# Optimization experiments

Hardware: AMD Instinct MI355X
Metric: run time of the kernel (lower is better)

The kernel has to match this reference:

```python
import jax, jax.numpy as jnp
import numpy as np

NUM_HEADS = 16
BLOCK_SIZE = 64
NUM_GLOBAL_TOKENS = 64
WINDOW_SIZE = 256
NUM_RANDOM_BLOCKS = 3
BATCH = 2
SEQ_LEN = 4096
EMBED_DIM = 1024


def _alibi_slopes(n):
    # power-of-2 head count path of _compute_alibi_slopes
    base = 2.0 ** (-(2.0 ** (-(np.log2(n) - 3.0))))
    return jnp.asarray([base ** i for i in range(1, n + 1)], dtype=jnp.float32)


def _build_block_indices():
    nb = SEQ_LEN // BLOCK_SIZE
    ngb = NUM_GLOBAL_TOKENS // BLOCK_SIZE
    wb = WINDOW_SIZE // BLOCK_SIZE
    mb = 2 * wb + 1 + NUM_RANDOM_BLOCKS
    rng = np.random.default_rng(0)
    out = np.full((nb, mb), -1, dtype=np.int64)
    for qb in range(nb):
        attended = set(range(ngb))  # global blocks handled separately
        idx = 0
        for kb in range(max(ngb, qb - wb), min(nb, qb + wb + 1)):
            if kb not in attended:
                out[qb, idx] = kb
                attended.add(kb)
                idx += 1
        cand = [b for b in range(ngb, nb) if b not in attended]
        pick = rng.choice(len(cand), size=min(NUM_RANDOM_BLOCKS, len(cand)), replace=False)
        for j in pick:
            out[qb, idx] = cand[j]
            idx += 1
    return jnp.asarray(out)


def setup_inputs() -> dict:
    key = jax.random.key(0)
    ks = jax.random.split(key, 5)
    s = 0.02
    x = jax.random.normal(ks[0], (BATCH, SEQ_LEN, EMBED_DIM), jnp.float32)
    Wq = jax.random.normal(ks[1], (EMBED_DIM, EMBED_DIM), jnp.float32) * s
    Wk = jax.random.normal(ks[2], (EMBED_DIM, EMBED_DIM), jnp.float32) * s
    Wv = jax.random.normal(ks[3], (EMBED_DIM, EMBED_DIM), jnp.float32) * s
    Wo = jax.random.normal(ks[4], (EMBED_DIM, EMBED_DIM), jnp.float32) * s
    return {"x": x, "Wq": Wq, "Wk": Wk, "Wv": Wv, "Wo": Wo,
            "block_indices": _build_block_indices()}


def reference(x, Wq, Wk, Wv, Wo, block_indices):
    B, S, E = x.shape
    H = NUM_HEADS
    Dh = E // H
    G = NUM_GLOBAL_TOKENS
    BS = BLOCK_SIZE
    scale = 1.0 / np.sqrt(Dh)

    def split_heads(t):
        return t.reshape(B, S, H, Dh).transpose(0, 2, 1, 3)  # [B,H,S,Dh]

    q = split_heads(x @ Wq)
    k = split_heads(x @ Wk)
    v = split_heads(x @ Wv)

    slopes = _alibi_slopes(H)  # [H]
    pos = jnp.arange(S, dtype=jnp.float32)

    # ---- global tokens: full attention over all keys ----
    sg = jnp.einsum('bhgd,bhsd->bhgs', q[:, :, :G], k) * scale
    bias_g = -slopes[:, None, None] * jnp.abs(pos[:G, None] - pos[None, :])  # [H,G,S]
    pg = jax.nn.softmax(sg + bias_g[None], axis=-1)
    out_g = jnp.einsum('bhgs,bhsd->bhgd', pg, v)  # [B,H,G,Dh]

    # ---- sparse queries: global KV + gathered sparse blocks ----
    nb = S // BS
    ngb = G // BS
    nqb = nb - ngb
    bi = block_indices[ngb:]           # [nqb, MB], -1 = padding
    mb = bi.shape[1]
    bsafe = jnp.maximum(bi, 0)

    kb = k.reshape(B, H, nb, BS, Dh)
    vb = v.reshape(B, H, nb, BS, Dh)
    kg = kb[:, :, bsafe].reshape(B, H, nqb, mb * BS, Dh)
    vg = vb[:, :, bsafe].reshape(B, H, nqb, mb * BS, Dh)
    kglob = jnp.broadcast_to(k[:, :, None, :G], (B, H, nqb, G, Dh))
    vglob = jnp.broadcast_to(v[:, :, None, :G], (B, H, nqb, G, Dh))
    kcat = jnp.concatenate([kglob, kg], axis=3)  # [B,H,nqb,G+mb*BS,Dh]
    vcat = jnp.concatenate([vglob, vg], axis=3)

    qn = q[:, :, G:].reshape(B, H, nqb, BS, Dh)
    scores = jnp.einsum('bhqmd,bhqnd->bhqmn', qn, kcat) * scale

    qpos = (G + jnp.arange(nqb * BS, dtype=jnp.float32)).reshape(nqb, BS)
    loc_pos = (bsafe[:, :, None] * BS + jnp.arange(BS)[None, None, :]).reshape(nqb, mb * BS).astype(jnp.float32)
    kpos = jnp.concatenate([jnp.broadcast_to(pos[:G][None], (nqb, G)), loc_pos], axis=1)
    bias = -slopes[:, None, None, None] * jnp.abs(qpos[None, :, :, None] - kpos[None, :, None, :])  # [H,nqb,BS,Kt]

    valid = jnp.concatenate([jnp.ones((nqb, G), bool), jnp.repeat(bi >= 0, BS, axis=1)], axis=1)
    scores = jnp.where(valid[None, None, :, None, :], scores + bias[None], -jnp.inf)
    p = jax.nn.softmax(scores, axis=-1)
    out_s = jnp.einsum('bhqmn,bhqnd->bhqmd', p, vcat).reshape(B, H, S - G, Dh)

    out = jnp.concatenate([out_g, out_s], axis=2)  # [B,H,S,Dh]
    out = out.transpose(0, 2, 1, 3).reshape(B, S, E)
    return out @ Wo
```

## Files before the change

### kernel.cpp

```cpp
#include <hip/hip_runtime.h>
#include <stdint.h>

typedef __attribute__((ext_vector_type(8))) short short8;
typedef __attribute__((ext_vector_type(4))) float f32x4;
typedef __attribute__((ext_vector_type(8))) unsigned short u16x8;

#define DEV static __device__ __forceinline__

DEV unsigned short f2bf(float f) {
  union { float f; uint32_t u; } v; v.f = f;
  uint32_t r = v.u + 0x7FFFu + ((v.u >> 16) & 1u);
  return (unsigned short)(r >> 16);
}

DEV void gload16(const void* g, void* l) {
  __builtin_amdgcn_global_load_lds(
      (const __attribute__((address_space(1))) void*)g,
      (__attribute__((address_space(3))) void*)l, 16, 0, 0);
}

__global__ void cast_x_kernel(const float* __restrict__ x, unsigned short* __restrict__ xb) {
  int i = blockIdx.x * 256 + threadIdx.x;
  f32x4 a = ((const f32x4*)x)[2 * i];
  f32x4 b = ((const f32x4*)x)[2 * i + 1];
  u16x8 o;
  o[0] = f2bf(a[0]); o[1] = f2bf(a[1]); o[2] = f2bf(a[2]); o[3] = f2bf(a[3]);
  o[4] = f2bf(b[0]); o[5] = f2bf(b[1]); o[6] = f2bf(b[2]); o[7] = f2bf(b[3]);
  ((u16x8*)xb)[i] = o;
}

__global__ void transpose_w_kernel(const float* __restrict__ Wq, const float* __restrict__ Wk,
                                   const float* __restrict__ Wv, const float* __restrict__ Wo,
                                   unsigned short* __restrict__ wt) {
  __shared__ float tile[64][65];
  int z = blockIdx.z;
  const float* W = (z == 0) ? Wq : (z == 1) ? Wk : (z == 2) ? Wv : Wo;
  unsigned short* dst = wt + (size_t)z * 1024 * 1024;
  int bn = blockIdx.x, bk = blockIdx.y;
  int t = threadIdx.x;
  int c = t & 63, rr = t >> 6;
#pragma unroll
  for (int p = 0; p < 16; ++p) {
    int r = p * 4 + rr;
    tile[r][c] = W[(size_t)(bk * 64 + r) * 1024 + bn * 64 + c];
  }
  __syncthreads();
#pragma unroll
  for (int p = 0; p < 16; ++p) {
    int r2 = p * 4 + rr;
    dst[(size_t)(bn * 64 + r2) * 1024 + bk * 64 + c] = f2bf(tile[c][r2]);
  }
}

__global__ __launch_bounds__(256, 2) void gemm_qkv(const unsigned short* __restrict__ A,
                                                   const unsigned short* __restrict__ wt,
                                                   unsigned short* __restrict__ Qb,
                                                   unsigned short* __restrict__ Kb,
                                                   unsigned short* __restrict__ Vtb,
                                                   float qscale) {
  constexpr int K = 1024;
  __shared__ __align__(16) unsigned short As[128 * 64];
  __shared__ __align__(16) unsigned short Bs[128 * 64];
  int bn = blockIdx.x, bm = blockIdx.y;
  int which = bn >> 3, bnn = bn & 7;
  int tid = threadIdx.x, lane = tid & 63, w = tid >> 6;
  int wr = w >> 1, wc = w & 1;
  f32x4 acc[4][4] = {};

  int sr[4], soff[4];
#pragma unroll
  for (int i = 0; i < 4; ++i) {
    int ci = w * 4 + i;
    int r = ci * 8 + (lane >> 3);
    sr[i] = r;
    soff[i] = ((lane & 7) ^ (r & 7)) * 8;
  }
  const unsigned short* Arow = A + (size_t)(bm * 128) * K;
  const unsigned short* Brow = wt + (size_t)which * 1048576 + (size_t)(bnn * 128) * K;

  for (int k0 = 0; k0 < K; k0 += 64) {
#pragma unroll
    for (int i = 0; i < 4; ++i) {
      gload16(Arow + (size_t)sr[i] * K + k0 + soff[i], As + (w * 4 + i) * 512);
      gload16(Brow + (size_t)sr[i] * K + k0 + soff[i], Bs + (w * 4 + i) * 512);
    }
    __syncthreads();
    short8 af[2][4], bfr[2][4];
#pragma unroll
    for (int c = 0; c < 2; ++c) {
#pragma unroll
      for (int m = 0; m < 4; ++m) {
        int cc = (lane >> 4) + 4 * c;
        int ra = wr * 64 + m * 16 + (lane & 15);
        af[c][m] = *(const short8*)(As + ra * 64 + ((cc ^ (ra & 7)) * 8));
        int rb = wc * 64 + m * 16 + (lane & 15);
        bfr[c][m] = *(const short8*)(Bs + rb * 64 + ((cc ^ (rb & 7)) * 8));
      }
    }
#pragma unroll
    for (int c = 0; c < 2; ++c)
#pragma unroll
      for (int m = 0; m < 4; ++m)
#pragma unroll
        for (int n = 0; n < 4; ++n)
          acc[m][n] = __builtin_amdgcn_mfma_f32_16x16x32_bf16(af[c][m], bfr[c][n], acc[m][n], 0, 0, 0);
    __syncthreads();
  }

  int rbase = bm * 128 + wr * 64;
  int cbase = bnn * 128 + wc * 64;
#pragma unroll
  for (int m = 0; m < 4; ++m)
#pragma unroll
    for (int n = 0; n < 4; ++n) {
      int row0 = rbase + m * 16 + (lane >> 4) * 4;
      int col = cbase + n * 16 + (lane & 15);
      int h = col >> 6, d = col & 63;
#pragma unroll
      for (int reg = 0; reg < 4; ++reg) {
        int row = row0 + reg;
        float v = acc[m][n][reg];
        int b = row >> 12, s = row & 4095;
        if (which == 0)
          Qb[((size_t)(b * 16 + h) * 4096 + s) * 64 + d] = f2bf(v * qscale);
        else if (which == 1)
          Kb[((size_t)(b * 16 + h) * 4096 + s) * 64 + d] = f2bf(v);
        else
          Vtb[(((size_t)(b * 16 + h) * 64 + (s >> 6)) * 64 + d) * 64 + (s & 63)] = f2bf(v);
      }
    }
}

__global__ __launch_bounds__(256, 2) void gemm_out(const unsigned short* __restrict__ A,
                                                   const unsigned short* __restrict__ Bt,
                                                   float* __restrict__ dst) {
  constexpr int K = 1024;
  __shared__ __align__(16) unsigned short As[128 * 64];
  __shared__ __align__(16) unsigned short Bs[128 * 64];
  int bn = blockIdx.x, bm = blockIdx.y;
  int tid = threadIdx.x, lane = tid & 63, w = tid >> 6;
  int wr = w >> 1, wc = w & 1;
  f32x4 acc[4][4] = {};

  int sr[4], soff[4];
#pragma unroll
  for (int i = 0; i < 4; ++i) {
    int ci = w * 4 + i;
    int r = ci * 8 + (lane >> 3);
    sr[i] = r;
    soff[i] = ((lane & 7) ^ (r & 7)) * 8;
  }
  const unsigned short* Arow = A + (size_t)(bm * 128) * K;
  const unsigned short* Brow = Bt + (size_t)(bn * 128) * K;

  for (int k0 = 0; k0 < K; k0 += 64) {
#pragma unroll
    for (int i = 0; i < 4; ++i) {
      gload16(Arow + (size_t)sr[i] * K + k0 + soff[i], As + (w * 4 + i) * 512);
      gload16(Brow + (size_t)sr[i] * K + k0 + soff[i], Bs + (w * 4 + i) * 512);
    }
    __syncthreads();
    short8 af[2][4], bfr[2][4];
#pragma unroll
    for (int c = 0; c < 2; ++c) {
#pragma unroll
      for (int m = 0; m < 4; ++m) {
        int cc = (lane >> 4) + 4 * c;
        int ra = wr * 64 + m * 16 + (lane & 15);
        af[c][m] = *(const short8*)(As + ra * 64 + ((cc ^ (ra & 7)) * 8));
        int rb = wc * 64 + m * 16 + (lane & 15);
        bfr[c][m] = *(const short8*)(Bs + rb * 64 + ((cc ^ (rb & 7)) * 8));
      }
    }
#pragma unroll
    for (int c = 0; c < 2; ++c)
#pragma unroll
      for (int m = 0; m < 4; ++m)
#pragma unroll
        for (int n = 0; n < 4; ++n)
          acc[m][n] = __builtin_amdgcn_mfma_f32_16x16x32_bf16(af[c][m], bfr[c][n], acc[m][n], 0, 0, 0);
    __syncthreads();
  }

  int rbase = bm * 128 + wr * 64;
  int cbase = bn * 128 + wc * 64;
#pragma unroll
  for (int m = 0; m < 4; ++m)
#pragma unroll
    for (int n = 0; n < 4; ++n) {
      int row0 = rbase + m * 16 + (lane >> 4) * 4;
      int col = cbase + n * 16 + (lane & 15);
#pragma unroll
      for (int reg = 0; reg < 4; ++reg)
        dst[(size_t)(row0 + reg) * 1024 + col] = acc[m][n][reg];
    }
}

__global__ __launch_bounds__(256) void attn_kernel(const unsigned short* __restrict__ Qh,
                            const unsigned short* __restrict__ Kh,
                            const unsigned short* __restrict__ Vbt,
                            const int* __restrict__ bidx,
                            unsigned short* __restrict__ attn_out,
                            float* __restrict__ Opart,
                            float* __restrict__ lpart) {
  __shared__ __align__(16) unsigned short Ks[2][64 * 64];
  __shared__ __align__(16) unsigned short Vs[2][64 * 64];
  __shared__ __align__(16) unsigned short Pl[2][4][16][72];
  int flat = blockIdx.x + 71 * blockIdx.y;
  int nf = (flat & 7) * 284 + (flat >> 3);
  int gx = nf % 71, bh = nf / 71;
  int h = bh & 15;
  int tid = threadIdx.x, lane = tid & 63, w = tid >> 6;
  float slope2 = exp2f(-0.5f * (float)(h + 1)) * 1.44269504f;

  int qb, nkb;
  int list[13];
  if (gx < 63) {
    qb = gx + 1;
    nkb = 1;
    list[0] = 0;
#pragma unroll
    for (int j = 0; j < 12; ++j) {
      int v = bidx[qb * 12 + j];
      if (v >= 0) list[nkb++] = v;
    }
  } else {
    qb = 0;
    int chunk = gx - 63;
    nkb = 8;
#pragma unroll
    for (int i = 0; i < 8; ++i) list[i] = chunk * 8 + i;
  }

  int qrow = qb * 64 + w * 16 + (lane & 15);
  const unsigned short* qptr = Qh + ((size_t)bh * 4096 + qrow) * 64 + (lane >> 4) * 8;
  short8 qf0 = *(const short8*)qptr;
  short8 qf1 = *(const short8*)(qptr + 32);

  float psum[4] = {0.f, 0.f, 0.f, 0.f};
  f32x4 accO[4] = {};
  int qpos0 = qb * 64 + w * 16 + (lane >> 4) * 4;

  float qposf[4], fm[4], fp[4], kctf[4];
#pragma unroll
  for (int reg = 0; reg < 4; ++reg) {
    qposf[reg] = (float)(qpos0 + reg);
    fm[reg] = -slope2 * qposf[reg];
    fp[reg] = slope2 * qposf[reg];
  }
#pragma unroll
  for (int ct = 0; ct < 4; ++ct) kctf[ct] = (float)(ct * 16 + (lane & 15));

  const unsigned short* Kbh = Kh + (size_t)bh * 4096 * 64;
  const unsigned short* Vbh = Vbt + (size_t)bh * 4096 * 64;

  int sr[2], so[2];
#pragma unroll
  for (int i = 0; i < 2; ++i) {
    int ci = w * 2 + i;
    int r = ci * 8 + (lane >> 3);
    sr[i] = r;
    so[i] = ((lane & 7) ^ (r & 7)) * 8;
  }
  auto STAGE = [&](int bi, int kb) {
    const unsigned short* kbase = Kbh + (size_t)kb * 4096;
    const unsigned short* vbase = Vbh + (size_t)kb * 4096;
#pragma unroll
    for (int i = 0; i < 2; ++i) {
      gload16(kbase + sr[i] * 64 + so[i], &Ks[bi][(w * 2 + i) * 512]);
      gload16(vbase + sr[i] * 64 + so[i], &Vs[bi][(w * 2 + i) * 512]);
    }
  };

  STAGE(0, list[0]);

  for (int it = 0; it < nkb; ++it) {
    int cur = it & 1;
    int kb = list[it];
    __syncthreads();
    if (it + 1 < nkb) STAGE(cur ^ 1, list[it + 1]);

    float kbf = (float)(kb * 64);
    float skb = slope2 * kbf;
    float pv[4][4];

    if (kb != qb) {
      float d_[4][4];
      if (kb < qb) {
#pragma unroll
        for (int ct = 0; ct < 4; ++ct) {
          float e = __builtin_fmaf(slope2, kctf[ct], skb);
#pragma unroll
          for (int reg = 0; reg < 4; ++reg) d_[ct][reg] = fm[reg] + e;
        }
      } else {
#pragma unroll
        for (int ct = 0; ct < 4; ++ct) {
          float e = __builtin_fmaf(slope2, kctf[ct], skb);
#pragma unroll
          for (int reg = 0; reg < 4; ++reg) d_[ct][reg] = fp[reg] - e;
        }
      }
      __builtin_amdgcn_s_setprio(1);
#pragma unroll
      for (int ct = 0; ct < 4; ++ct) {
        int kr = ct * 16 + (lane & 15);
        short8 kf0 = *(const short8*)(&Ks[cur][kr * 64 + (((lane >> 4) ^ (kr & 7)) * 8)]);
        short8 kf1 = *(const short8*)(&Ks[cur][kr * 64 + ((((lane >> 4) + 4) ^ (kr & 7)) * 8)]);
        f32x4 s = __builtin_amdgcn_mfma_f32_16x16x32_bf16(qf0, kf0, (f32x4){0.f, 0.f, 0.f, 0.f}, 0, 0, 0);
        s = __builtin_amdgcn_mfma_f32_16x16x32_bf16(qf1, kf1, s, 0, 0, 0);
#pragma unroll
        for (int reg = 0; reg < 4; ++reg) {
          float p = exp2f(s[reg] + d_[ct][reg]);
          pv[ct][reg] = p;
          psum[reg] += p;
        }
      }
      __builtin_amdgcn_s_setprio(0);
    } else {
      float qmb[4];
#pragma unroll
      for (int reg = 0; reg < 4; ++reg) qmb[reg] = qposf[reg] - kbf;
      __builtin_amdgcn_s_setprio(1);
#pragma unroll
      for (int ct = 0; ct < 4; ++ct) {
        int kr = ct * 16 + (lane & 15);
        short8 kf0 = *(const short8*)(&Ks[cur][kr * 64 + (((lane >> 4) ^ (kr & 7)) * 8)]);
        short8 kf1 = *(const short8*)(&Ks[cur][kr * 64 + ((((lane >> 4) + 4) ^ (kr & 7)) * 8)]);
        f32x4 s = __builtin_amdgcn_mfma_f32_16x16x32_bf16(qf0, kf0, (f32x4){0.f, 0.f, 0.f, 0.f}, 0, 0, 0);
        s = __builtin_amdgcn_mfma_f32_16x16x32_bf16(qf1, kf1, s, 0, 0, 0);
#pragma unroll
        for (int reg = 0; reg < 4; ++reg) {
          float diff = qmb[reg] - kctf[ct];
          float p = exp2f(__builtin_fmaf(-slope2, fabsf(diff), s[reg]));
          pv[ct][reg] = p;
          psum[reg] += p;
        }
      }
      __builtin_amdgcn_s_setprio(0);
    }

#pragma unroll
    for (int cp = 0; cp < 2; ++cp)
#pragma unroll
      for (int reg = 0; reg < 4; ++reg) {
        uint32_t pk;
        asm("v_cvt_pk_bf16_f32 %0, %1, %2" : "=v"(pk) : "v"(pv[2 * cp][reg]), "v"(pv[2 * cp + 1][reg]));
        int row = (lane >> 4) * 4 + reg;
        int c = lane & 15;
        Pl[cur][w][row][cp * 32 + c] = (unsigned short)pk;
        Pl[cur][w][row][cp * 32 + 16 + c] = (unsigned short)(pk >> 16);
      }

    asm volatile("s_waitcnt lgkmcnt(0)" ::: "memory");
    short8 pa0 = *(const short8*)(&Pl[cur][w][lane & 15][(lane >> 4) * 8]);
    short8 pa1 = *(const short8*)(&Pl[cur][w][lane & 15][(lane >> 4) * 8 + 32]);
    __builtin_amdgcn_s_setprio(1);
#pragma unroll
    for (int dt = 0; dt < 4; ++dt) {
      int dr = dt * 16 + (lane & 15);
      short8 vf0 = *(const short8*)(&Vs[cur][dr * 64 + (((lane >> 4) ^ (dr & 7)) * 8)]);
      short8 vf1 = *(const short8*)(&Vs[cur][dr * 64 + ((((lane >> 4) + 4) ^ (dr & 7)) * 8)]);
      accO[dt] = __builtin_amdgcn_mfma_f32_16x16x32_bf16(pa0, vf0, accO[dt], 0, 0, 0);
      accO[dt] = __builtin_amdgcn_mfma_f32_16x16x32_bf16(pa1, vf1, accO[dt], 0, 0, 0);
    }
    __builtin_amdgcn_s_setprio(0);
  }

  float l[4];
#pragma unroll
  for (int reg = 0; reg < 4; ++reg) {
    float v = psum[reg];
#pragma unroll
    for (int off = 1; off < 16; off <<= 1) v += __shfl_xor(v, off, 64);
    l[reg] = v;
  }

  int b = bh >> 4;
  if (gx < 63) {
#pragma unroll
    for (int reg = 0; reg < 4; ++reg) {
      float rl = 1.0f / l[reg];
#pragma unroll
      for (int dt = 0; dt < 4; ++dt) {
        int row = qb * 64 + w * 16 + (lane >> 4) * 4 + reg;
        int col = h * 64 + dt * 16 + (lane & 15);
        attn_out[((size_t)b * 4096 + row) * 1024 + col] = f2bf(accO[dt][reg] * rl);
      }
    }
  } else {
    int chunk = gx - 63;
    float* Op = Opart + (size_t)(bh * 8 + chunk) * 64 * 64;
    float* lp = lpart + (size_t)(bh * 8 + chunk) * 64;
#pragma unroll
    for (int reg = 0; reg < 4; ++reg) {
      int row = w * 16 + (lane >> 4) * 4 + reg;
#pragma unroll
      for (int dt = 0; dt < 4; ++dt) {
        int col = dt * 16 + (lane & 15);
        Op[row * 64 + col] = accO[dt][reg];
      }
      if ((lane & 15) == 0) lp[row] = l[reg];
    }
  }
}

__global__ void merge_qb0(const float* __restrict__ Opart, const float* __restrict__ lpart,
                          unsigned short* __restrict__ attn_out) {
  int bh = blockIdx.x;
  int tid = threadIdx.x;
  int row = tid >> 2, cg = tid & 3;
  const float* lp = lpart + (size_t)bh * 8 * 64;
  float L = 0.f;
#pragma unroll
  for (int c = 0; c < 8; ++c) L += lp[c * 64 + row];
  float rL = 1.0f / L;
  int b = bh >> 4, h = bh & 15;
  f32x4 acc0 = {}, acc1 = {}, acc2 = {}, acc3 = {};
#pragma unroll
  for (int c = 0; c < 8; ++c) {
    const float* Op = Opart + ((size_t)(bh * 8 + c) * 64 + row) * 64 + cg * 16;
    acc0 += ((const f32x4*)Op)[0];
    acc1 += ((const f32x4*)Op)[1];
    acc2 += ((const f32x4*)Op)[2];
    acc3 += ((const f32x4*)Op)[3];
  }
  unsigned short* out = attn_out + ((size_t)b * 4096 + row) * 1024 + h * 64 + cg * 16;
#pragma unroll
  for (int j = 0; j < 4; ++j) {
    out[j] = f2bf(acc0[j] * rL);
    out[4 + j] = f2bf(acc1[j] * rL);
    out[8 + j] = f2bf(acc2[j] * rL);
    out[12 + j] = f2bf(acc3[j] * rL);
  }
}

extern "C" void kernel_launch(void* const* d_in, const int* in_sizes, int n_in,
                              void* d_out, int out_size, void* d_ws, size_t ws_size,
                              hipStream_t stream) {
  const float* x = (const float*)d_in[0];
  const float* Wq = (const float*)d_in[1];
  const float* Wk = (const float*)d_in[2];
  const float* Wv = (const float*)d_in[3];
  const float* Wo = (const float*)d_in[4];
  const int* bidx = (const int*)d_in[5];

  char* ws = (char*)d_ws;
  unsigned short* xb = (unsigned short*)(ws);
  unsigned short* wt = (unsigned short*)(ws + 16777216);
  unsigned short* Qb = (unsigned short*)(ws + 25165824);
  unsigned short* Kb = (unsigned short*)(ws + 41943040);
  unsigned short* Vtb = (unsigned short*)(ws + 58720256);
  unsigned short* attnb = (unsigned short*)(ws + 75497472);
  float* Opart = (float*)(ws);
  float* lpart = (float*)(ws + 4194304);

  cast_x_kernel<<<4096, 256, 0, stream>>>(x, xb);
  transpose_w_kernel<<<dim3(16, 16, 4), 256, 0, stream>>>(Wq, Wk, Wv, Wo, wt);
  gemm_qkv<<<dim3(24, 64), 256, 0, stream>>>(xb, wt, Qb, Kb, Vtb, 0.18033688f);
  attn_kernel<<<dim3(71, 32), 256, 0, stream>>>(Qb, Kb, Vtb, bidx, attnb, Opart, lpart);
  merge_qb0<<<32, 256, 0, stream>>>(Opart, lpart, attnb);
  gemm_out<<<dim3(8, 64), 256, 0, stream>>>(attnb, wt + 3145728, (float*)d_out);
}
```

Baseline: 189.9 us.

## Double-buffer GEMM LDS tiles, remap blocks per XCD, pack V-transpose stores

Both the QKV and output-projection GEMMs now use two LDS buffers, so the next K-tile is loaded while MFMAs run on the current one. Explicit vmcnt waits and raw barriers replace __syncthreads. Block indices are remapped so blocks sharing a weight column slice land on the same XCD, for better L2 reuse. The V-transposed epilogue packs four bf16 values with v_cvt_pk_bf16_f32 into one 8-byte store; the trade is doubled LDS use, which may lower occupancy.

```diff
diff --git a/kernel.cpp b/kernel.cpp
--- a/kernel.cpp
+++ b/kernel.cpp
@@ -4,6 +4,7 @@
 typedef __attribute__((ext_vector_type(8))) short short8;
 typedef __attribute__((ext_vector_type(4))) float f32x4;
 typedef __attribute__((ext_vector_type(8))) unsigned short u16x8;
+typedef __attribute__((ext_vector_type(2))) unsigned int u32x2;
 
 #define DEV static __device__ __forceinline__
 
@@ -59,9 +60,12 @@
                                                    unsigned short* __restrict__ Vtb,
                                                    float qscale) {
   constexpr int K = 1024;
-  __shared__ __align__(16) unsigned short As[128 * 64];
-  __shared__ __align__(16) unsigned short Bs[128 * 64];
-  int bn = blockIdx.x, bm = blockIdx.y;
+  __shared__ __align__(16) unsigned short As[2][128 * 64];
+  __shared__ __align__(16) unsigned short Bs[2][128 * 64];
+  int flat = blockIdx.x + 24 * blockIdx.y;
+  int xcd = flat & 7, idx = flat >> 3;
+  int bn = xcd * 3 + idx % 3;
+  int bm = idx / 3;
   int which = bn >> 3, bnn = bn & 7;
   int tid = threadIdx.x, lane = tid & 63, w = tid >> 6;
   int wr = w >> 1, wc = w & 1;
@@ -78,13 +82,25 @@
   const unsigned short* Arow = A + (size_t)(bm * 128) * K;
   const unsigned short* Brow = wt + (size_t)which * 1048576 + (size_t)(bnn * 128) * K;
 
-  for (int k0 = 0; k0 < K; k0 += 64) {
+  auto STAGE = [&](int bi, int k0) {
 #pragma unroll
     for (int i = 0; i < 4; ++i) {
-      gload16(Arow + (size_t)sr[i] * K + k0 + soff[i], As + (w * 4 + i) * 512);
-      gload16(Brow + (size_t)sr[i] * K + k0 + soff[i], Bs + (w * 4 + i) * 512);
-    }
-    __syncthreads();
+      gload16(Arow + (size_t)sr[i] * K + k0 + soff[i], &As[bi][(w * 4 + i) * 512]);
+      gload16(Brow + (size_t)sr[i] * K + k0 + soff[i], &Bs[bi][(w * 4 + i) * 512]);
+    }
+  };
+
+  STAGE(0, 0);
+  for (int kt = 0; kt < 16; ++kt) {
+    int cur = kt & 1;
+    if (kt < 15) {
+      STAGE(cur ^ 1, (kt + 1) * 64);
+      asm volatile("s_waitcnt vmcnt(8)" ::: "memory");
+    } else {
+      asm volatile("s_waitcnt vmcnt(0)" ::: "memory");
+    }
+    __builtin_amdgcn_s_barrier();
+    __builtin_amdgcn_sched_barrier(0);
     short8 af[2][4], bfr[2][4];
 #pragma unroll
     for (int c = 0; c < 2; ++c) {
@@ -92,9 +108,9 @@
       for (int m = 0; m < 4; ++m) {
         int cc = (lane >> 4) + 4 * c;
         int ra = wr * 64 + m * 16 + (lane & 15);
-        af[c][m] = *(const short8*)(As + ra * 64 + ((cc ^ (ra & 7)) * 8));
+        af[c][m] = *(const short8*)(&As[cur][ra * 64 + ((cc ^ (ra & 7)) * 8)]);
         int rb = wc * 64 + m * 16 + (lane & 15);
-        bfr[c][m] = *(const short8*)(Bs + rb * 64 + ((cc ^ (rb & 7)) * 8));
+        bfr[c][m] = *(const short8*)(&Bs[cur][rb * 64 + ((cc ^ (rb & 7)) * 8)]);
       }
     }
 #pragma unroll
@@ -104,7 +120,8 @@
 #pragma unroll
         for (int n = 0; n < 4; ++n)
           acc[m][n] = __builtin_amdgcn_mfma_f32_16x16x32_bf16(af[c][m], bfr[c][n], acc[m][n], 0, 0, 0);
-    __syncthreads();
+    __builtin_amdgcn_s_barrier();
+    __builtin_amdgcn_sched_barrier(0);
   }
 
   int rbase = bm * 128 + wr * 64;
@@ -116,17 +133,20 @@
       int row0 = rbase + m * 16 + (lane >> 4) * 4;
       int col = cbase + n * 16 + (lane & 15);
       int h = col >> 6, d = col & 63;
-#pragma unroll
-      for (int reg = 0; reg < 4; ++reg) {
-        int row = row0 + reg;
-        float v = acc[m][n][reg];
-        int b = row >> 12, s = row & 4095;
-        if (which == 0)
-          Qb[((size_t)(b * 16 + h) * 4096 + s) * 64 + d] = f2bf(v * qscale);
-        else if (which == 1)
-          Kb[((size_t)(b * 16 + h) * 4096 + s) * 64 + d] = f2bf(v);
-        else
-          Vtb[(((size_t)(b * 16 + h) * 64 + (s >> 6)) * 64 + d) * 64 + (s & 63)] = f2bf(v);
+      int b = row0 >> 12, s0 = row0 & 4095;
+      if (which == 0) {
+#pragma unroll
+        for (int reg = 0; reg < 4; ++reg)
+          Qb[((size_t)(b * 16 + h) * 4096 + s0 + reg) * 64 + d] = f2bf(acc[m][n][reg] * qscale);
+      } else if (which == 1) {
+#pragma unroll
+        for (int reg = 0; reg < 4; ++reg)
+          Kb[((size_t)(b * 16 + h) * 4096 + s0 + reg) * 64 + d] = f2bf(acc[m][n][reg]);
+      } else {
+        u32x2 pk;
+        asm("v_cvt_pk_bf16_f32 %0, %1, %2" : "=v"(pk[0]) : "v"(acc[m][n][0]), "v"(acc[m][n][1]));
+        asm("v_cvt_pk_bf16_f32 %0, %1, %2" : "=v"(pk[1]) : "v"(acc[m][n][2]), "v"(acc[m][n][3]));
+        *(u32x2*)(Vtb + ((((size_t)(b * 16 + h) * 64 + (s0 >> 6)) * 64 + d) * 64 + (s0 & 63))) = pk;
       }
     }
 }
@@ -135,9 +155,12 @@
                                                    const unsigned short* __restrict__ Bt,
                                                    float* __restrict__ dst) {
   constexpr int K = 1024;
-  __shared__ __align__(16) unsigned short As[128 * 64];
-  __shared__ __align__(16) unsigned short Bs[128 * 64];
-  int bn = blockIdx.x, bm = blockIdx.y;
+  __shared__ __align__(16) unsigned short As[2][128 * 64];
+  __shared__ __align__(16) unsigned short Bs[2][128 * 64];
+  int flat = blockIdx.x + 8 * blockIdx.y;
+  int xcd = flat & 7, idx = flat >> 3;
+  int bn = xcd;
+  int bm = idx;
   int tid = threadIdx.x, lane = tid & 63, w = tid >> 6;
   int wr = w >> 1, wc = w & 1;
   f32x4 acc[4][4] = {};
@@ -153,13 +176,25 @@
   const unsigned short* Arow = A + (size_t)(bm * 128) * K;
   const unsigned short* Brow = Bt + (size_t)(bn * 128) * K;
 
-  for (int k0 = 0; k0 < K; k0 += 64) {
+  auto STAGE = [&](int bi, int k0) {
 #pragma unroll
     for (int i = 0; i < 4; ++i) {
-      gload16(Arow + (size_t)sr[i] * K + k0 + soff[i], As + (w * 4 + i) * 512);
-      gload16(Brow + (size_t)sr[i] * K + k0 + soff[i], Bs + (w * 4 + i) * 512);
-    }
-    __syncthreads();
+      gload16(Arow + (size_t)sr[i] * K + k0 + soff[i], &As[bi][(w * 4 + i) * 512]);
+      gload16(Brow + (size_t)sr[i] * K + k0 + soff[i], &Bs[bi][(w * 4 + i) * 512]);
+    }
+  };
+
+  STAGE(0, 0);
+  for (int kt = 0; kt < 16; ++kt) {
+    int cur = kt & 1;
+    if (kt < 15) {
+      STAGE(cur ^ 1, (kt + 1) * 64);
+      asm volatile("s_waitcnt vmcnt(8)" ::: "memory");
+    } else {
+      asm volatile("s_waitcnt vmcnt(0)" ::: "memory");
+    }
+    __builtin_amdgcn_s_barrier();
+    __builtin_amdgcn_sched_barrier(0);
     short8 af[2][4], bfr[2][4];
 #pragma unroll
     for (int c = 0; c < 2; ++c) {
@@ -167,9 +202,9 @@
       for (int m = 0; m < 4; ++m) {
         int cc = (lane >> 4) + 4 * c;
         int ra = wr * 64 + m * 16 + (lane & 15);
-        af[c][m] = *(const short8*)(As + ra * 64 + ((cc ^ (ra & 7)) * 8));
+        af[c][m] = *(const short8*)(&As[cur][ra * 64 + ((cc ^ (ra & 7)) * 8)]);
         int rb = wc * 64 + m * 16 + (lane & 15);
-        bfr[c][m] = *(const short8*)(Bs + rb * 64 + ((cc ^ (rb & 7)) * 8));
+        bfr[c][m] = *(const short8*)(&Bs[cur][rb * 64 + ((cc ^ (rb & 7)) * 8)]);
       }
     }
 #pragma unroll
@@ -179,7 +214,8 @@
 #pragma unroll
         for (int n = 0; n < 4; ++n)
           acc[m][n] = __builtin_amdgcn_mfma_f32_16x16x32_bf16(af[c][m], bfr[c][n], acc[m][n], 0, 0, 0);
-    __syncthreads();
+    __builtin_amdgcn_s_barrier();
+    __builtin_amdgcn_sched_barrier(0);
   }
 
   int rbase = bm * 128 + wr * 64;
```

After: 178.7 us. -5.9%, faster.
